# Optimization experiments

Measured on AMD Instinct MI355X. Metric: run time of the kernel, lower is better.

The kernel has to match this reference:

```python
import jax, jax.numpy as jnp
import numpy as np

EPS = 1e-6
TEMP = 1.0
L = 64  # shapelet_len


def _znorm(a):
    # z-normalize over last axis, population std, clamped by EPS (matches torch unbiased=False + clamp_min)
    mean = a.mean(axis=-1, keepdims=True)
    std = jnp.maximum(a.std(axis=-1, keepdims=True), EPS)
    return (a - mean) / std


def setup_inputs() -> dict:
    key = jax.random.key(0)
    k1, k2 = jax.random.split(key)
    bs, T, C, P = 32, 8192, 1, 64
    x = jax.random.normal(k1, (bs, T, C), dtype=jnp.float32)
    shapelets = jax.random.normal(k2, (P, C, L), dtype=jnp.float32)
    return {"x": x, "shapelets": shapelets}


def reference(x, shapelets):
    # x: [bs, T, C]; shapelets: [P, C, L]
    bs, T, C = x.shape
    P = shapelets.shape[0]
    x_ct = jnp.transpose(x, (0, 2, 1))  # [bs, C, T]
    Tp = T - L + 1
    # sliding windows: [bs, C, T', L]
    idx = jnp.arange(Tp)[:, None] + jnp.arange(L)[None, :]
    w = x_ct[:, :, idx]
    # z-normalize windows and shapelets over the length axis
    w = _znorm(w)
    s = _znorm(shapelets)
    # squared euclidean distance via expansion ||w||^2 - 2 w.s + ||s||^2 (sum over C and L)
    w2 = jnp.sum(w * w, axis=(1, 3))          # [bs, T']
    s2 = jnp.sum(s * s, axis=(1, 2))          # [P]
    dot = jnp.einsum('bctl,pcl->btp', w, s)   # [bs, T', P]
    dist2 = w2[:, :, None] + s2[None, None, :] - 2.0 * dot
    temp = max(TEMP, EPS)
    act = jnp.exp(-dist2 / temp)              # [bs, T', P]
    # center-pad to length T: left = L//2, right = T - (T' + left)
    left = L // 2
    right = max(0, T - (Tp + left))
    act_full = jnp.pad(act, ((0, 0), (left, right), (0, 0)))
    return act_full[:, :T, :]
```

## Files before the change

kernel.cpp:

```cpp
#include <hip/hip_runtime.h>
#include <math.h>

#define T_LEN 8192
#define EPSF  1e-6f

typedef __attribute__((ext_vector_type(8))) short short8;
typedef __attribute__((ext_vector_type(4))) float float4v;

__global__ __launch_bounds__(64) void prep_kernel(const float* __restrict__ sh,
                                                  unsigned short* __restrict__ bhi,
                                                  unsigned short* __restrict__ blo,
                                                  float* __restrict__ snsum,
                                                  float* __restrict__ s2) {
    int p = threadIdx.x;
    float v[64];
    float s1 = 0.f;
#pragma unroll
    for (int l = 0; l < 64; ++l) { v[l] = sh[p * 64 + l]; s1 += v[l]; }
    float mu = s1 * (1.f / 64.f);
    float sq = 0.f;
#pragma unroll
    for (int l = 0; l < 64; ++l) { float d = v[l] - mu; sq = fmaf(d, d, sq); }
    float sd  = fmaxf(sqrtf(sq * (1.f / 64.f)), EPSF);
    float inv = 1.f / sd;
    float ssum = 0.f, ss2 = 0.f;
#pragma unroll
    for (int l = 0; l < 64; ++l) {
        float s = (v[l] - mu) * inv;
        unsigned ub = __float_as_uint(s);
        unsigned hb = ub & 0xFFFF0000u;
        float hi = __uint_as_float(hb);
        float lo = s - hi;
        unsigned lb = __float_as_uint(lo) & 0xFFFF0000u;
        bhi[p * 64 + l] = (unsigned short)(ub >> 16);
        blo[p * 64 + l] = (unsigned short)(__float_as_uint(lo) >> 16);
        float eff = hi + __uint_as_float(lb);
        ssum += eff;
        ss2  = fmaf(eff, eff, ss2);
    }
    snsum[p] = ssum;
    s2[p]    = ss2;
}

__global__ __launch_bounds__(256, 3) void shapelet_mfma(
        const float* __restrict__ x,
        const unsigned short* __restrict__ gbhi,
        const unsigned short* __restrict__ gblo,
        const float* __restrict__ gsum,
        const float* __restrict__ gs2,
        float* __restrict__ out) {
    __shared__ unsigned short Bhi[64][72];
    __shared__ unsigned short Blo[64][72];
    __shared__ float xs[192];
    __shared__ float lmu[128], linv[128], lw2[128];
    __shared__ float lsum[64], ls2[64];

    const int tid  = threadIdx.x;
    const int lane = tid & 63;
    const int wave = tid >> 6;
    const int n    = lane & 15;
    const int quad = lane >> 4;

    const int super = blockIdx.x & 63;
    const int b     = blockIdx.x >> 6;
    const int t0    = super << 7;

    const float4* gh4 = (const float4*)gbhi;
    const float4* gl4 = (const float4*)gblo;
#pragma unroll
    for (int i = 0; i < 2; ++i) {
        int idx = tid + (i << 8);
        int p = idx >> 3, k0 = (idx & 7) << 3;
        *(float4*)&Bhi[p][k0] = gh4[idx];
        *(float4*)&Blo[p][k0] = gl4[idx];
    }
    if (tid < 64) { lsum[tid] = gsum[tid]; ls2[tid] = gs2[tid]; }
    if (tid < 192) {
        int g = t0 - 32 + tid;
        xs[tid] = ((unsigned)g < (unsigned)T_LEN) ? x[(size_t)b * T_LEN + g] : 0.f;
    }
    __syncthreads();

    short8 Bh[4][2], Bl[4][2];
#pragma unroll
    for (int pt = 0; pt < 4; ++pt)
#pragma unroll
        for (int h = 0; h < 2; ++h) {
            Bh[pt][h] = *(const short8*)&Bhi[pt * 16 + n][h * 32 + (quad << 3)];
            Bl[pt][h] = *(const short8*)&Blo[pt * 16 + n][h * 32 + (quad << 3)];
        }

    if (tid < 128) {
        float s1 = 0.f, sq = 0.f;
#pragma unroll
        for (int l = 0; l < 64; ++l) { float v = xs[tid + l]; s1 += v; sq = fmaf(v, v, sq); }
        float mu  = s1 * (1.f / 64.f);
        float var = fmaxf(sq * (1.f / 64.f) - mu * mu, 0.f);
        float sd  = fmaxf(sqrtf(var), EPSF);
        float inv = 1.f / sd;
        lmu[tid]  = mu;
        linv[tid] = inv;
        lw2[tid]  = 64.f * var * inv * inv;
    }
    __syncthreads();

#pragma unroll
    for (int u = 0; u < 2; ++u) {
        const int abase = (u << 6) + (wave << 4) + n + (quad << 3);
        short8 Ah[2], Al[2];
#pragma unroll
        for (int h = 0; h < 2; ++h) {
#pragma unroll
            for (int j = 0; j < 8; ++j) {
                float v = xs[abase + h * 32 + j];
                unsigned ub = __float_as_uint(v);
                unsigned hb = ub & 0xFFFF0000u;
                float lo = v - __uint_as_float(hb);
                Ah[h][j] = (short)(ub >> 16);
                Al[h][j] = (short)(__float_as_uint(lo) >> 16);
            }
        }

        float4v acc[4];
#pragma unroll
        for (int pt = 0; pt < 4; ++pt) {
            float4v a = {0.f, 0.f, 0.f, 0.f};
#pragma unroll
            for (int h = 0; h < 2; ++h) {
                a = __builtin_amdgcn_mfma_f32_16x16x32_bf16(Ah[h], Bh[pt][h], a, 0, 0, 0);
                a = __builtin_amdgcn_mfma_f32_16x16x32_bf16(Ah[h], Bl[pt][h], a, 0, 0, 0);
                a = __builtin_amdgcn_mfma_f32_16x16x32_bf16(Al[h], Bh[pt][h], a, 0, 0, 0);
            }
            acc[pt] = a;
        }

        float sm[4], sv[4];
#pragma unroll
        for (int pt = 0; pt < 4; ++pt) { sm[pt] = lsum[pt * 16 + n]; sv[pt] = ls2[pt * 16 + n]; }
#pragma unroll
        for (int r = 0; r < 4; ++r) {
            int tl = (u << 6) + (wave << 4) + (quad << 2) + r;
            int tg = t0 + tl;
            bool valid = (tg >= 32) && (tg <= 8160);
            float mu  = lmu[tl];
            float inv = linv[tl];
            float w2  = lw2[tl];
            float* orow = out + ((size_t)(b * T_LEN + tg) << 6);
#pragma unroll
            for (int pt = 0; pt < 4; ++pt) {
                float dot  = (acc[pt][r] - mu * sm[pt]) * inv;
                float dist = w2 + sv[pt] - 2.f * dot;
                orow[pt * 16 + n] = valid ? __expf(-dist) : 0.f;
            }
        }
    }
}

extern "C" void kernel_launch(void* const* d_in, const int* in_sizes, int n_in,
                              void* d_out, int out_size, void* d_ws, size_t ws_size,
                              hipStream_t stream) {
    const float* x  = (const float*)d_in[0];
    const float* sh = (const float*)d_in[1];
    float* out = (float*)d_out;

    unsigned short* bhi = (unsigned short*)d_ws;
    unsigned short* blo = bhi + 64 * 64;
    float* snsum = (float*)(blo + 64 * 64);
    float* s2v   = snsum + 64;

    prep_kernel<<<1, 64, 0, stream>>>(sh, bhi, blo, snsum, s2v);
    shapelet_mfma<<<32 * 64, 256, 0, stream>>>(x, bhi, blo, snsum, s2v, out);
}
```

Measured before the change: 86.47 us.

## Fuse shapelet normalization prep into main MFMA kernel, drop separate launch

```diff
diff --git a/kernel.cpp b/kernel.cpp
--- a/kernel.cpp
+++ b/kernel.cpp
@@ -7,48 +7,11 @@
 typedef __attribute__((ext_vector_type(8))) short short8;
 typedef __attribute__((ext_vector_type(4))) float float4v;
 
-__global__ __launch_bounds__(64) void prep_kernel(const float* __restrict__ sh,
-                                                  unsigned short* __restrict__ bhi,
-                                                  unsigned short* __restrict__ blo,
-                                                  float* __restrict__ snsum,
-                                                  float* __restrict__ s2) {
-    int p = threadIdx.x;
-    float v[64];
-    float s1 = 0.f;
-#pragma unroll
-    for (int l = 0; l < 64; ++l) { v[l] = sh[p * 64 + l]; s1 += v[l]; }
-    float mu = s1 * (1.f / 64.f);
-    float sq = 0.f;
-#pragma unroll
-    for (int l = 0; l < 64; ++l) { float d = v[l] - mu; sq = fmaf(d, d, sq); }
-    float sd  = fmaxf(sqrtf(sq * (1.f / 64.f)), EPSF);
-    float inv = 1.f / sd;
-    float ssum = 0.f, ss2 = 0.f;
-#pragma unroll
-    for (int l = 0; l < 64; ++l) {
-        float s = (v[l] - mu) * inv;
-        unsigned ub = __float_as_uint(s);
-        unsigned hb = ub & 0xFFFF0000u;
-        float hi = __uint_as_float(hb);
-        float lo = s - hi;
-        unsigned lb = __float_as_uint(lo) & 0xFFFF0000u;
-        bhi[p * 64 + l] = (unsigned short)(ub >> 16);
-        blo[p * 64 + l] = (unsigned short)(__float_as_uint(lo) >> 16);
-        float eff = hi + __uint_as_float(lb);
-        ssum += eff;
-        ss2  = fmaf(eff, eff, ss2);
-    }
-    snsum[p] = ssum;
-    s2[p]    = ss2;
-}
-
-__global__ __launch_bounds__(256, 3) void shapelet_mfma(
+__global__ __launch_bounds__(256, 4) void shapelet_fused(
         const float* __restrict__ x,
-        const unsigned short* __restrict__ gbhi,
-        const unsigned short* __restrict__ gblo,
-        const float* __restrict__ gsum,
-        const float* __restrict__ gs2,
+        const float* __restrict__ sh,
         float* __restrict__ out) {
+    __shared__ float Sraw[64][65];
     __shared__ unsigned short Bhi[64][72];
     __shared__ unsigned short Blo[64][72];
     __shared__ float xs[192];
@@ -65,19 +28,84 @@
     const int b     = blockIdx.x >> 6;
     const int t0    = super << 7;
 
-    const float4* gh4 = (const float4*)gbhi;
-    const float4* gl4 = (const float4*)gblo;
+    {
+        const float4* g4 = (const float4*)sh;
 #pragma unroll
-    for (int i = 0; i < 2; ++i) {
-        int idx = tid + (i << 8);
-        int p = idx >> 3, k0 = (idx & 7) << 3;
-        *(float4*)&Bhi[p][k0] = gh4[idx];
-        *(float4*)&Blo[p][k0] = gl4[idx];
+        for (int i = 0; i < 4; ++i) {
+            int idx = tid + (i << 8);
+            float4 v = g4[idx];
+            int e = idx << 2;
+            int row = e >> 6, col = e & 63;
+            Sraw[row][col + 0] = v.x;
+            Sraw[row][col + 1] = v.y;
+            Sraw[row][col + 2] = v.z;
+            Sraw[row][col + 3] = v.w;
+        }
+        if (tid < 192) {
+            int g = t0 - 32 + tid;
+            xs[tid] = ((unsigned)g < (unsigned)T_LEN) ? x[(size_t)b * T_LEN + g] : 0.f;
+        }
     }
-    if (tid < 64) { lsum[tid] = gsum[tid]; ls2[tid] = gs2[tid]; }
-    if (tid < 192) {
-        int g = t0 - 32 + tid;
-        xs[tid] = ((unsigned)g < (unsigned)T_LEN) ? x[(size_t)b * T_LEN + g] : 0.f;
+    __syncthreads();
+
+    if (tid < 64) {
+        const int p = tid;
+        float s1 = 0.f;
+        for (int l = 0; l < 64; ++l) s1 += Sraw[p][l];
+        float mu = s1 * (1.f / 64.f);
+        float sq = 0.f;
+        for (int l = 0; l < 64; ++l) { float d = Sraw[p][l] - mu; sq = fmaf(d, d, sq); }
+        float sd  = fmaxf(sqrtf(sq * (1.f / 64.f)), EPSF);
+        float inv = 1.f / sd;
+        float ssum = 0.f, ss2 = 0.f;
+        for (int l2 = 0; l2 < 32; ++l2) {
+            unsigned pk_h, pk_l;
+            {
+                float v = Sraw[p][2 * l2];
+                float s = (v - mu) * inv;
+                unsigned ub = __float_as_uint(s);
+                float hi = __uint_as_float(ub & 0xFFFF0000u);
+                float lo = s - hi;
+                unsigned lb = __float_as_uint(lo) & 0xFFFF0000u;
+                pk_h = ub >> 16;
+                pk_l = lb >> 16;
+                float eff = hi + __uint_as_float(lb);
+                ssum += eff;
+                ss2  = fmaf(eff, eff, ss2);
+            }
+            {
+                float v = Sraw[p][2 * l2 + 1];
+                float s = (v - mu) * inv;
+                unsigned ub = __float_as_uint(s);
+                float hi = __uint_as_float(ub & 0xFFFF0000u);
+                float lo = s - hi;
+                unsigned lb = __float_as_uint(lo) & 0xFFFF0000u;
+                pk_h |= (ub & 0xFFFF0000u);
+                pk_l |= lb;
+                float eff = hi + __uint_as_float(lb);
+                ssum += eff;
+                ss2  = fmaf(eff, eff, ss2);
+            }
+            *(unsigned*)&Bhi[p][2 * l2] = pk_h;
+            *(unsigned*)&Blo[p][2 * l2] = pk_l;
+        }
+        lsum[p] = ssum;
+        ls2[p]  = ss2;
+    } else if (tid < 192) {
+        const int r = tid - 64;
+        float s1 = 0.f, sq = 0.f;
+#pragma unroll
+        for (int l = 0; l < 64; ++l) {
+            float v = xs[r + l];
+            s1 += v; sq = fmaf(v, v, sq);
+        }
+        float mu  = s1 * (1.f / 64.f);
+        float var = fmaxf(sq * (1.f / 64.f) - mu * mu, 0.f);
+        float sd  = fmaxf(sqrtf(var), EPSF);
+        float inv = 1.f / sd;
+        lmu[r]  = mu;
+        linv[r] = inv;
+        lw2[r]  = 64.f * var * inv * inv;
     }
     __syncthreads();
 
@@ -89,20 +117,6 @@
             Bh[pt][h] = *(const short8*)&Bhi[pt * 16 + n][h * 32 + (quad << 3)];
             Bl[pt][h] = *(const short8*)&Blo[pt * 16 + n][h * 32 + (quad << 3)];
         }
-
-    if (tid < 128) {
-        float s1 = 0.f, sq = 0.f;
-#pragma unroll
-        for (int l = 0; l < 64; ++l) { float v = xs[tid + l]; s1 += v; sq = fmaf(v, v, sq); }
-        float mu  = s1 * (1.f / 64.f);
-        float var = fmaxf(sq * (1.f / 64.f) - mu * mu, 0.f);
-        float sd  = fmaxf(sqrtf(var), EPSF);
-        float inv = 1.f / sd;
-        lmu[tid]  = mu;
-        linv[tid] = inv;
-        lw2[tid]  = 64.f * var * inv * inv;
-    }
-    __syncthreads();
 
 #pragma unroll
     for (int u = 0; u < 2; ++u) {
@@ -163,11 +177,5 @@
     const float* sh = (const float*)d_in[1];
     float* out = (float*)d_out;
 
-    unsigned short* bhi = (unsigned short*)d_ws;
-    unsigned short* blo = bhi + 64 * 64;
-    float* snsum = (float*)(blo + 64 * 64);
-    float* s2v   = snsum + 64;
-
-    prep_kernel<<<1, 64, 0, stream>>>(sh, bhi, blo, snsum, s2v);
-    shapelet_mfma<<<32 * 64, 256, 0, stream>>>(x, bhi, blo, snsum, s2v, out);
+    shapelet_fused<<<32 * 64, 256, 0, stream>>>(x, sh, out);
 }
```

Measured after the change: 85.23 us. Within noise of the previous version (-1.4%).

## Pre-swizzle shapelet fragments and permute columns for vectorized float4 output stores

Applied to the files above, without the earlier changes.

```diff
diff --git a/kernel.cpp b/kernel.cpp
--- a/kernel.cpp
+++ b/kernel.cpp
@@ -8,32 +8,31 @@
 typedef __attribute__((ext_vector_type(4))) float float4v;
 
 __global__ __launch_bounds__(64) void prep_kernel(const float* __restrict__ sh,
-                                                  unsigned short* __restrict__ bhi,
-                                                  unsigned short* __restrict__ blo,
+                                                  unsigned short* __restrict__ fbhi,
+                                                  unsigned short* __restrict__ fblo,
                                                   float* __restrict__ snsum,
                                                   float* __restrict__ s2) {
-    int p = threadIdx.x;
+    const int p = threadIdx.x;
+    const int n = p >> 2, pt = p & 3;
     float v[64];
     float s1 = 0.f;
-#pragma unroll
     for (int l = 0; l < 64; ++l) { v[l] = sh[p * 64 + l]; s1 += v[l]; }
     float mu = s1 * (1.f / 64.f);
     float sq = 0.f;
-#pragma unroll
     for (int l = 0; l < 64; ++l) { float d = v[l] - mu; sq = fmaf(d, d, sq); }
     float sd  = fmaxf(sqrtf(sq * (1.f / 64.f)), EPSF);
     float inv = 1.f / sd;
     float ssum = 0.f, ss2 = 0.f;
-#pragma unroll
     for (int l = 0; l < 64; ++l) {
         float s = (v[l] - mu) * inv;
         unsigned ub = __float_as_uint(s);
-        unsigned hb = ub & 0xFFFF0000u;
-        float hi = __uint_as_float(hb);
+        float hi = __uint_as_float(ub & 0xFFFF0000u);
         float lo = s - hi;
         unsigned lb = __float_as_uint(lo) & 0xFFFF0000u;
-        bhi[p * 64 + l] = (unsigned short)(ub >> 16);
-        blo[p * 64 + l] = (unsigned short)(__float_as_uint(lo) >> 16);
+        int h = l >> 5, quad = (l >> 3) & 3, j = l & 7;
+        int idx = (((pt * 2 + h) * 4 + quad) * 16 + n) * 8 + j;
+        fbhi[idx] = (unsigned short)(ub >> 16);
+        fblo[idx] = (unsigned short)(lb >> 16);
         float eff = hi + __uint_as_float(lb);
         ssum += eff;
         ss2  = fmaf(eff, eff, ss2);
@@ -42,18 +41,15 @@
     s2[p]    = ss2;
 }
 
-__global__ __launch_bounds__(256, 3) void shapelet_mfma(
+__global__ __launch_bounds__(256, 4) void shapelet_mfma(
         const float* __restrict__ x,
-        const unsigned short* __restrict__ gbhi,
-        const unsigned short* __restrict__ gblo,
+        const unsigned short* __restrict__ fbhi,
+        const unsigned short* __restrict__ fblo,
         const float* __restrict__ gsum,
         const float* __restrict__ gs2,
         float* __restrict__ out) {
-    __shared__ unsigned short Bhi[64][72];
-    __shared__ unsigned short Blo[64][72];
     __shared__ float xs[192];
     __shared__ float lmu[128], linv[128], lw2[128];
-    __shared__ float lsum[64], ls2[64];
 
     const int tid  = threadIdx.x;
     const int lane = tid & 63;
@@ -65,42 +61,54 @@
     const int b     = blockIdx.x >> 6;
     const int t0    = super << 7;
 
-    const float4* gh4 = (const float4*)gbhi;
-    const float4* gl4 = (const float4*)gblo;
+    short8 Bh[4][2], Bl[4][2];
+    {
+        const short8* gh = (const short8*)fbhi;
+        const short8* gl = (const short8*)fblo;
 #pragma unroll
-    for (int i = 0; i < 2; ++i) {
-        int idx = tid + (i << 8);
-        int p = idx >> 3, k0 = (idx & 7) << 3;
-        *(float4*)&Bhi[p][k0] = gh4[idx];
-        *(float4*)&Blo[p][k0] = gl4[idx];
+        for (int pt = 0; pt < 4; ++pt)
+#pragma unroll
+            for (int h = 0; h < 2; ++h) {
+                int idx = ((pt * 2 + h) * 4 + quad) * 16 + n;
+                Bh[pt][h] = gh[idx];
+                Bl[pt][h] = gl[idx];
+            }
     }
-    if (tid < 64) { lsum[tid] = gsum[tid]; ls2[tid] = gs2[tid]; }
-    if (tid < 192) {
-        int g = t0 - 32 + tid;
-        xs[tid] = ((unsigned)g < (unsigned)T_LEN) ? x[(size_t)b * T_LEN + g] : 0.f;
+    const float4 sm4 = *(const float4*)(gsum + (n << 2));
+    const float4 sv4 = *(const float4*)(gs2  + (n << 2));
+
+    if (tid < 48) {
+        int g0 = t0 - 32 + (tid << 2);
+        float4 v;
+        if (g0 >= 0 && g0 + 3 < T_LEN) {
+            v = *(const float4*)(x + (size_t)b * T_LEN + g0);
+        } else {
+            float* vp = (float*)&v;
+#pragma unroll
+            for (int e = 0; e < 4; ++e) {
+                int g = g0 + e;
+                vp[e] = ((unsigned)g < (unsigned)T_LEN) ? x[(size_t)b * T_LEN + g] : 0.f;
+            }
+        }
+        *(float4*)&xs[tid << 2] = v;
     }
     __syncthreads();
 
-    short8 Bh[4][2], Bl[4][2];
-#pragma unroll
-    for (int pt = 0; pt < 4; ++pt)
-#pragma unroll
-        for (int h = 0; h < 2; ++h) {
-            Bh[pt][h] = *(const short8*)&Bhi[pt * 16 + n][h * 32 + (quad << 3)];
-            Bl[pt][h] = *(const short8*)&Blo[pt * 16 + n][h * 32 + (quad << 3)];
-        }
-
     if (tid < 128) {
+        const int r = tid;
         float s1 = 0.f, sq = 0.f;
 #pragma unroll
-        for (int l = 0; l < 64; ++l) { float v = xs[tid + l]; s1 += v; sq = fmaf(v, v, sq); }
+        for (int l = 0; l < 64; ++l) {
+            float v = xs[r + l];
+            s1 += v; sq = fmaf(v, v, sq);
+        }
         float mu  = s1 * (1.f / 64.f);
         float var = fmaxf(sq * (1.f / 64.f) - mu * mu, 0.f);
         float sd  = fmaxf(sqrtf(var), EPSF);
         float inv = 1.f / sd;
-        lmu[tid]  = mu;
-        linv[tid] = inv;
-        lw2[tid]  = 64.f * var * inv * inv;
+        lmu[r]  = mu;
+        linv[r] = inv;
+        lw2[r]  = 64.f * var * inv * inv;
     }
     __syncthreads();
 
@@ -134,9 +142,6 @@
             acc[pt] = a;
         }
 
-        float sm[4], sv[4];
-#pragma unroll
-        for (int pt = 0; pt < 4; ++pt) { sm[pt] = lsum[pt * 16 + n]; sv[pt] = ls2[pt * 16 + n]; }
 #pragma unroll
         for (int r = 0; r < 4; ++r) {
             int tl = (u << 6) + (wave << 4) + (quad << 2) + r;
@@ -145,13 +150,16 @@
             float mu  = lmu[tl];
             float inv = linv[tl];
             float w2  = lw2[tl];
-            float* orow = out + ((size_t)(b * T_LEN + tg) << 6);
-#pragma unroll
-            for (int pt = 0; pt < 4; ++pt) {
-                float dot  = (acc[pt][r] - mu * sm[pt]) * inv;
-                float dist = w2 + sv[pt] - 2.f * dot;
-                orow[pt * 16 + n] = valid ? __expf(-dist) : 0.f;
-            }
+            float d0 = (acc[0][r] - mu * sm4.x) * inv;
+            float d1 = (acc[1][r] - mu * sm4.y) * inv;
+            float d2 = (acc[2][r] - mu * sm4.z) * inv;
+            float d3 = (acc[3][r] - mu * sm4.w) * inv;
+            float4 o;
+            o.x = valid ? __expf(-(w2 + sv4.x - 2.f * d0)) : 0.f;
+            o.y = valid ? __expf(-(w2 + sv4.y - 2.f * d1)) : 0.f;
+            o.z = valid ? __expf(-(w2 + sv4.z - 2.f * d2)) : 0.f;
+            o.w = valid ? __expf(-(w2 + sv4.w - 2.f * d3)) : 0.f;
+            *(float4*)(out + (((size_t)(b * T_LEN + tg)) << 6) + (n << 2)) = o;
         }
     }
 }
@@ -163,11 +171,11 @@
     const float* sh = (const float*)d_in[1];
     float* out = (float*)d_out;
 
-    unsigned short* bhi = (unsigned short*)d_ws;
-    unsigned short* blo = bhi + 64 * 64;
-    float* snsum = (float*)(blo + 64 * 64);
+    unsigned short* fbhi = (unsigned short*)d_ws;
+    unsigned short* fblo = fbhi + 64 * 64;
+    float* snsum = (float*)(fblo + 64 * 64);
     float* s2v   = snsum + 64;
 
-    prep_kernel<<<1, 64, 0, stream>>>(sh, bhi, blo, snsum, s2v);
-    shapelet_mfma<<<32 * 64, 256, 0, stream>>>(x, bhi, blo, snsum, s2v, out);
+    prep_kernel<<<1, 64, 0, stream>>>(sh, fbhi, fblo, snsum, s2v);
+    shapelet_mfma<<<32 * 64, 256, 0, stream>>>(x, fbhi, fblo, snsum, s2v, out);
 }
```

Result: no change. 87.74 us (+1.5%).
